# Optimization experiments

Hardware: AMD Instinct MI355X
Metric: run time of the kernel (lower is better)

The kernel has to match this reference:

```python
import jax, jax.numpy as jnp
import numpy as np

H = W = 128
BS = 16
# Ragged per-canvas stroke counts (sum = 2048)
LENGTHS = np.array([64, 192, 128, 96, 160, 224, 32, 128, 128, 256, 64, 96, 160, 128, 96, 96], dtype=np.int64)
L = int(LENGTHS.sum())


def setup_inputs() -> dict:
    key = jax.random.key(0)
    k1, k2, k3 = jax.random.split(key, 3)
    u = jax.random.uniform(k1, (L, 8), dtype=jnp.float32)
    # keep stroke width/height in [0.1, 0.6] so 1/w, 1/h stay well-conditioned
    strokes = u.at[:, 2:4].set(0.1 + 0.5 * u[:, 2:4])
    meta_brushes = jax.random.uniform(k2, (2, 1, H, W), dtype=jnp.float32)
    start_canvas = jax.random.uniform(k3, (BS, 3, H, W), dtype=jnp.float32)
    return {"strokes": strokes, "meta_brushes": meta_brushes,
            "start_canvas": start_canvas, "lengths": LENGTHS}


def _grid_sample_bilinear(img, gx, gy):
    """torch.nn.functional.grid_sample(mode='bilinear', padding_mode='zeros',
    align_corners=False) for single-channel images.
    img: [L, H, W]; gx, gy: [L, Ho, Wo] normalized coords in [-1, 1]."""
    Lb, Hi, Wi = img.shape
    ix = (gx + 1.0) * (Wi * 0.5) - 0.5
    iy = (gy + 1.0) * (Hi * 0.5) - 0.5
    x0 = jnp.floor(ix)
    y0 = jnp.floor(iy)
    x1 = x0 + 1.0
    y1 = y0 + 1.0
    wx1 = ix - x0
    wx0 = 1.0 - wx1
    wy1 = iy - y0
    wy0 = 1.0 - wy1
    bidx = jnp.arange(Lb)[:, None, None]

    def tap(xf, yf):
        xi = jnp.clip(xf, 0, Wi - 1).astype(jnp.int32)
        yi = jnp.clip(yf, 0, Hi - 1).astype(jnp.int32)
        valid = (xf >= 0) & (xf <= Wi - 1) & (yf >= 0) & (yf <= Hi - 1)
        return jnp.where(valid, img[bidx, yi, xi], 0.0)

    return (wy0 * wx0 * tap(x0, y0) + wy0 * wx1 * tap(x1, y0)
            + wy1 * wx0 * tap(x0, y1) + wy1 * wx1 * tap(x1, y1))


def _strokes2brushes(strokes, meta_brushes):
    """Per-stroke affine warp of the meta brush (affine_grid + grid_sample)."""
    x0, y0, w, h, theta = [strokes[:, i] for i in range(5)]
    colors = strokes[:, 5:8]  # [L, 3]
    idx = (h <= w).astype(jnp.int32)          # vertical vs horizontal brush
    imgs = meta_brushes[idx, 0]               # [L, H, W]

    rad = theta * jnp.pi
    s, c = jnp.sin(rad), jnp.cos(rad)
    w00 = c / w
    w01 = s * H / (W * w)
    w02 = (1 - 2 * x0) * w00 + (1 - 2 * y0) * w01
    w10 = -s * W / (H * h)
    w11 = c / h
    w12 = (1 - 2 * y0) * w11 - (1 - 2 * x0) * (-w10)

    # affine_grid(align_corners=False): pixel-center normalized coords
    xs = (2.0 * jnp.arange(W) + 1.0) / W - 1.0  # [W]
    ys = (2.0 * jnp.arange(H) + 1.0) / H - 1.0  # [H]
    gxb, gyb = jnp.meshgrid(xs, ys)             # [H, W] each
    gx = w00[:, None, None] * gxb + w01[:, None, None] * gyb + w02[:, None, None]
    gy = w10[:, None, None] * gxb + w11[:, None, None] * gyb + w12[:, None, None]

    brushes = _grid_sample_bilinear(imgs, gx, gy)  # [L, H, W]
    return colors, brushes


def _forward(strokes, meta_brushes, start_canvas, lengths):
    lengths = np.asarray(lengths)
    bs = len(lengths)
    colors, brushes = _strokes2brushes(strokes, meta_brushes)
    alphas = jnp.where(brushes <= 0.6, brushes, 1.0)  # [L, H, W]

    # Segmented reverse-cumsum (flip->cumsum->flip minus self), vectorized:
    # suffix_excl_i = seg_total - inclusive_prefix_i
    ends = np.cumsum(lengths)                 # [bs]
    starts = ends - lengths                   # [bs]
    seg = np.repeat(np.arange(bs), lengths)   # [L] static segment ids
    csum = jnp.cumsum(alphas, axis=0)         # [L, H, W]
    csum_pad = jnp.concatenate([jnp.zeros((1, H, W), csum.dtype), csum], axis=0)
    pre = csum_pad[starts]                    # [bs, H, W] cumsum before seg start
    totals = csum_pad[ends] - pre             # [bs, H, W] per-segment alpha sum
    suffix_excl = totals[seg] - (csum - pre[seg])

    b = jnp.clip(brushes - suffix_excl, 0.0, 1.0)  # [L, H, W]
    canvas = jax.ops.segment_sum(colors[:, :, None, None] * b[:, None],
                                 seg, num_segments=bs)  # [bs, 3, H, W]
    canvas_alpha = jnp.clip(totals, 0.0, 1.0)           # [bs, H, W]

    # F.interpolate to (H, W) is identity here (start_canvas already HxW)
    canvas = canvas + start_canvas * (1.0 - canvas_alpha[:, None])
    return canvas.astype(jnp.float32)


def reference(strokes, meta_brushes, start_canvas, lengths):
    return _forward(strokes, meta_brushes, start_canvas, lengths)
```

## Files before the change

kernel.cpp:

```cpp
#include <hip/hip_runtime.h>

#define HW_ 16384
#define BS_ 16

static __device__ __constant__ int g_start[BS_] = {
    0, 64, 256, 384, 480, 640, 864, 896,
    1024, 1152, 1408, 1472, 1568, 1728, 1856, 1952};
static __device__ __constant__ int g_len[BS_] = {
    64, 192, 128, 96, 160, 224, 32, 128,
    128, 256, 64, 96, 160, 128, 96, 96};
static __device__ __constant__ int g_perm[BS_] = {
    9, 5, 1, 12, 4, 2, 7, 8, 0, 3, 11, 13, 6, 10, 14, 15};

__global__ __launch_bounds__(256) void light_render_kernel(
    const float* __restrict__ strokes,
    const float* __restrict__ meta,
    const float* __restrict__ start_canvas,
    float* __restrict__ out)
{
    __shared__ float sc[256 * 12];
    __shared__ unsigned short slist[4 * 256];
    __shared__ int s_wcnt[4];

    const int b    = g_perm[blockIdx.x >> 6];
    const int tile = blockIdx.x & 63;
    const int tx = tile & 7, ty = tile >> 3;
    const int t    = threadIdx.x;
    const int lane = t & 63, wid = t >> 6;
    const int qx = wid & 1, qy = wid >> 1;
    const int c0p = (tx << 4) + (qx << 3);
    const int r0p = (ty << 4) + (qy << 3);
    const int col = c0p + (lane & 7);
    const int row = r0p + (lane >> 3);
    const int p   = (row << 7) + col;
    const int sg0 = g_start[b];
    const int len = g_len[b];

    const float cxb = (float)(32 * tx + 16) * 0.0078125f - 1.0f;
    const float cyb = (float)(32 * ty + 16) * 0.0078125f - 1.0f;
    const float exb = 15.0f / 128.0f;

    float d0=0,d1=0,d2=0,d3=0,d4=0,d5=0,d6=0,d7=0,d8=0,d9=0;
    bool keep = false;
    if (t < len) {
        const float4* sp = (const float4*)(strokes + (size_t)(sg0 + t) * 8);
        const float4 s0 = sp[0];
        const float4 s1 = sp[1];
        float sn, cs;
        sincosf(s1.x * 3.14159274101257324f, &sn, &cs);
        const float iw = 64.0f / s0.z;
        const float ih = 64.0f / s0.w;
        const float W00 = cs * iw, W01 = sn * iw;
        const float W10 = -sn * ih, W11 = cs * ih;
        const float ax = 1.0f - 2.0f * s0.x;
        const float ay = 1.0f - 2.0f * s0.y;
        const float W02 = fmaf(ax, W00, fmaf(ay, W01, 63.5f));
        const float W12 = fmaf(ay, W11, fmaf(ax, W10, 63.5f));
        const float cx = fmaf(W00, cxb, fmaf(W01, cyb, W02));
        const float cy = fmaf(W10, cxb, fmaf(W11, cyb, W12));
        const float rx = fabsf(W00) * exb + fabsf(W01) * exb;
        const float ry = fabsf(W10) * exb + fabsf(W11) * exb;
        keep = (fabsf(cx - 63.5f) <= 65.5f + rx) &&
               (fabsf(cy - 63.5f) <= 65.5f + ry);
        d0 = W00; d1 = W01; d2 = W02; d3 = W10; d4 = W11; d5 = W12;
        d6 = s1.y; d7 = s1.z; d8 = s1.w;
        d9 = (s0.w <= s0.z) ? 16384.0f : 0.0f;
    }
    const unsigned long long ball = __ballot(keep);
    const int pre = __popcll(ball & ((1ull << lane) - 1ull));
    if (lane == 0) s_wcnt[wid] = __popcll(ball);
    __syncthreads();
    int woff = 0;
    #pragma unroll
    for (int i = 0; i < 3; ++i) woff += (i < wid) ? s_wcnt[i] : 0;
    const int total = s_wcnt[0] + s_wcnt[1] + s_wcnt[2] + s_wcnt[3];
    if (keep) {
        float* dst = sc + (size_t)(woff + pre) * 12;
        dst[0]=d0; dst[1]=d1; dst[2]=d2;  dst[3]=d3; dst[4]=d4;  dst[5]=d5;
        dst[6]=d6; dst[7]=d7; dst[8]=d8;  dst[9]=d9; dst[10]=0.f; dst[11]=0.f;
    }
    __syncthreads();

    const float4* sv = (const float4*)sc;
    const float wcx = (float)(2 * c0p + 8) * 0.0078125f - 1.0f;
    const float wcy = (float)(2 * r0p + 8) * 0.0078125f - 1.0f;
    const float wex = 7.0f / 128.0f;
    unsigned short* wl = slist + (wid << 8);
    int wn = 0;
    for (int base = 0; base < total; base += 64) {
        const int k = base + lane;
        bool kp = false;
        if (k < total) {
            const float4 a0 = sv[k * 3];
            const float4 a1 = sv[k * 3 + 1];
            const float cx = fmaf(a0.x, wcx, fmaf(a0.y, wcy, a0.z));
            const float cy = fmaf(a0.w, wcx, fmaf(a1.x, wcy, a1.y));
            const float rx = fabsf(a0.x) * wex + fabsf(a0.y) * wex;
            const float ry = fabsf(a0.w) * wex + fabsf(a1.x) * wex;
            kp = (fabsf(cx - 63.5f) <= 65.5f + rx) &&
                 (fabsf(cy - 63.5f) <= 65.5f + ry);
        }
        const unsigned long long bl = __ballot(kp);
        if (kp) {
            const int pr = __popcll(bl & ((1ull << lane) - 1ull));
            wl[wn + pr] = (unsigned short)k;
        }
        wn += __popcll(bl);
    }

    const float gxb = (float)(2 * col + 1) * 0.0078125f - 1.0f;
    const float gyb = (float)(2 * row + 1) * 0.0078125f - 1.0f;

    float accR = 0.0f, accG = 0.0f, accB = 0.0f;
    float S = 0.0f;

    int j = wn - 1;
    float4 a0, a1, a2;
    if (j >= 0) {
        const int k = wl[j];
        a0 = sv[k*3]; a1 = sv[k*3+1]; a2 = sv[k*3+2];
    }
    while (j >= 0) {
        const int jn = j - 1;
        int kn = 0;
        if (jn >= 0) kn = wl[jn];
        const float4 c0 = a0, c1 = a1, c2 = a2;
        if (jn >= 0) {
            a0 = sv[kn*3]; a1 = sv[kn*3+1]; a2 = sv[kn*3+2];
        }

        const float ixf = fmaf(c0.x, gxb, fmaf(c0.y, gyb, c0.z));
        const float iyf = fmaf(c0.w, gxb, fmaf(c1.x, gyb, c1.y));
        const bool inside = (ixf > -1.0f) && (ixf < 128.0f) &&
                            (iyf > -1.0f) && (iyf < 128.0f);
        if (inside && (S < 1.0f)) {
            const float x0f = floorf(ixf), y0f = floorf(iyf);
            float wx1 = ixf - x0f, wy1 = iyf - y0f;
            float wx0 = 1.0f - wx1, wy0 = 1.0f - wy1;
            if (x0f < 0.0f)    wx0 = 0.0f;
            if (x0f > 126.0f)  wx1 = 0.0f;
            if (y0f < 0.0f)    wy0 = 0.0f;
            if (y0f > 126.0f)  wy1 = 0.0f;

            const int ix0 = (int)x0f, iy0 = (int)y0f;
            const int xi0 = max(ix0, 0), xi1 = min(ix0 + 1, 127);
            const int yi0 = max(iy0, 0), yi1 = min(iy0 + 1, 127);

            const float* img = meta + (int)c2.y;
            const int row0 = yi0 << 7, row1 = yi1 << 7;
            const float t00 = img[row0 + xi0];
            const float t01 = img[row0 + xi1];
            const float t10 = img[row1 + xi0];
            const float t11 = img[row1 + xi1];

            const float v = wy0 * fmaf(wx0, t00, wx1 * t01) +
                            wy1 * fmaf(wx0, t10, wx1 * t11);

            const float alpha = (v <= 0.6f) ? v : 1.0f;
            const float bb = fminf(fmaxf(v - S, 0.0f), 1.0f);
            accR = fmaf(c1.z, bb, accR);
            accG = fmaf(c1.w, bb, accG);
            accB = fmaf(c2.x, bb, accB);
            S += alpha;
        }
        if (__all(S >= 1.0f)) break;
        j = jn;
    }

    const float rem = 1.0f - fminf(S, 1.0f);
    const size_t base = ((size_t)b * 3) << 14;
    out[base + p]          = fmaf(start_canvas[base + p],          rem, accR);
    out[base + HW_ + p]    = fmaf(start_canvas[base + HW_ + p],    rem, accG);
    out[base + 2*HW_ + p]  = fmaf(start_canvas[base + 2*HW_ + p],  rem, accB);
}

extern "C" void kernel_launch(void* const* d_in, const int* in_sizes, int n_in,
                              void* d_out, int out_size, void* d_ws, size_t ws_size,
                              hipStream_t stream) {
    const float* strokes      = (const float*)d_in[0];
    const float* meta_brushes = (const float*)d_in[1];
    const float* start_canvas = (const float*)d_in[2];
    float* out = (float*)d_out;

    dim3 grid(BS_ * 64);
    dim3 block(256);
    light_render_kernel<<<grid, block, 0, stream>>>(strokes, meta_brushes,
                                                    start_canvas, out);
}
```

Measured before the change: 14.56 us.

## Precompute zero-padded 2x2 quad texture to fetch bilinear taps in one load

```diff
diff --git a/kernel.cpp b/kernel.cpp
--- a/kernel.cpp
+++ b/kernel.cpp
@@ -2,6 +2,8 @@
 
 #define HW_ 16384
 #define BS_ 16
+#define QW_ 129
+#define QIMG_ (QW_ * QW_)
 
 static __device__ __constant__ int g_start[BS_] = {
     0, 64, 256, 384, 480, 640, 864, 896,
@@ -12,9 +14,29 @@
 static __device__ __constant__ int g_perm[BS_] = {
     9, 5, 1, 12, 4, 2, 7, 8, 0, 3, 11, 13, 6, 10, 14, 15};
 
+__global__ __launch_bounds__(256) void quad_meta_kernel(
+    const float* __restrict__ meta, float4* __restrict__ Q)
+{
+    int i = blockIdx.x * 256 + threadIdx.x;
+    if (i >= 2 * QIMG_) return;
+    const int img = i / QIMG_, rem = i - img * QIMG_;
+    const int y = rem / QW_, x = rem - y * QW_;
+    const float* M = meta + img * HW_;
+    float q00 = 0.f, q01 = 0.f, q10 = 0.f, q11 = 0.f;
+    const bool rin0 = (y >= 1) && (y <= 128);
+    const bool rin1 = (y + 1 >= 1) && (y + 1 <= 128);
+    const bool cin0 = (x >= 1) && (x <= 128);
+    const bool cin1 = (x + 1 >= 1) && (x + 1 <= 128);
+    if (rin0 && cin0) q00 = M[((y - 1) << 7) + (x - 1)];
+    if (rin0 && cin1) q01 = M[((y - 1) << 7) + x];
+    if (rin1 && cin0) q10 = M[(y << 7) + (x - 1)];
+    if (rin1 && cin1) q11 = M[(y << 7) + x];
+    Q[i] = make_float4(q00, q01, q10, q11);
+}
+
 __global__ __launch_bounds__(256) void light_render_kernel(
     const float* __restrict__ strokes,
-    const float* __restrict__ meta,
+    const float4* __restrict__ Q,
     const float* __restrict__ start_canvas,
     float* __restrict__ out)
 {
@@ -64,7 +86,7 @@
                (fabsf(cy - 63.5f) <= 65.5f + ry);
         d0 = W00; d1 = W01; d2 = W02; d3 = W10; d4 = W11; d5 = W12;
         d6 = s1.y; d7 = s1.z; d8 = s1.w;
-        d9 = (s0.w <= s0.z) ? 16384.0f : 0.0f;
+        d9 = (s0.w <= s0.z) ? (float)QIMG_ : 0.0f;
     }
     const unsigned long long ball = __ballot(keep);
     const int pre = __popcll(ball & ((1ull << lane) - 1ull));
@@ -135,26 +157,12 @@
                             (iyf > -1.0f) && (iyf < 128.0f);
         if (inside && (S < 1.0f)) {
             const float x0f = floorf(ixf), y0f = floorf(iyf);
-            float wx1 = ixf - x0f, wy1 = iyf - y0f;
-            float wx0 = 1.0f - wx1, wy0 = 1.0f - wy1;
-            if (x0f < 0.0f)    wx0 = 0.0f;
-            if (x0f > 126.0f)  wx1 = 0.0f;
-            if (y0f < 0.0f)    wy0 = 0.0f;
-            if (y0f > 126.0f)  wy1 = 0.0f;
-
-            const int ix0 = (int)x0f, iy0 = (int)y0f;
-            const int xi0 = max(ix0, 0), xi1 = min(ix0 + 1, 127);
-            const int yi0 = max(iy0, 0), yi1 = min(iy0 + 1, 127);
-
-            const float* img = meta + (int)c2.y;
-            const int row0 = yi0 << 7, row1 = yi1 << 7;
-            const float t00 = img[row0 + xi0];
-            const float t01 = img[row0 + xi1];
-            const float t10 = img[row1 + xi0];
-            const float t11 = img[row1 + xi1];
-
-            const float v = wy0 * fmaf(wx0, t00, wx1 * t01) +
-                            wy1 * fmaf(wx0, t10, wx1 * t11);
+            const float wx1 = ixf - x0f, wy1 = iyf - y0f;
+            const float wx0 = 1.0f - wx1, wy0 = 1.0f - wy1;
+            const int xb = (int)x0f + 1, yb = (int)y0f + 1;
+            const float4 q = Q[(int)c2.y + yb * QW_ + xb];
+            const float v = wy0 * fmaf(wx0, q.x, wx1 * q.y) +
+                            wy1 * fmaf(wx0, q.z, wx1 * q.w);
 
             const float alpha = (v <= 0.6f) ? v : 1.0f;
             const float bb = fminf(fmaxf(v - S, 0.0f), 1.0f);
@@ -180,10 +188,13 @@
     const float* strokes      = (const float*)d_in[0];
     const float* meta_brushes = (const float*)d_in[1];
     const float* start_canvas = (const float*)d_in[2];
-    float* out = (float*)d_out;
+    float*  out = (float*)d_out;
+    float4* Qws = (float4*)d_ws;
+
+    quad_meta_kernel<<<(2 * QIMG_ + 255) / 256, 256, 0, stream>>>(meta_brushes, Qws);
 
     dim3 grid(BS_ * 64);
     dim3 block(256);
-    light_render_kernel<<<grid, block, 0, stream>>>(strokes, meta_brushes,
+    light_render_kernel<<<grid, block, 0, stream>>>(strokes, Qws,
                                                     start_canvas, out);
 }
```

Result: slower. 18.39 us (+26.3%).

## Split stroke sequence across waves with per-round alpha prefix exchange

Applied to the files above, without the earlier changes.

```diff
diff --git a/kernel.cpp b/kernel.cpp
--- a/kernel.cpp
+++ b/kernel.cpp
@@ -2,6 +2,7 @@
 
 #define HW_ 16384
 #define BS_ 16
+#define K_  16
 
 static __device__ __constant__ int g_start[BS_] = {
     0, 64, 256, 384, 480, 640, 864, 896,
@@ -10,7 +11,9 @@
     64, 192, 128, 96, 160, 224, 32, 128,
     128, 256, 64, 96, 160, 128, 96, 96};
 static __device__ __constant__ int g_perm[BS_] = {
-    9, 5, 1, 12, 4, 2, 7, 8, 0, 3, 11, 13, 6, 10, 14, 15};
+    9, 0, 4, 1, 12, 5, 2, 7, 3, 8, 11, 10, 14, 13, 6, 15};
+static __device__ __constant__ int g_txor[8] = {
+    0x00, 0x33, 0x55, 0x66, 0x99, 0xAA, 0xCC, 0xFF};
 
 __global__ __launch_bounds__(256) void light_render_kernel(
     const float* __restrict__ strokes,
@@ -18,29 +21,28 @@
     const float* __restrict__ start_canvas,
     float* __restrict__ out)
 {
-    __shared__ float sc[256 * 12];
-    __shared__ unsigned short slist[4 * 256];
-    __shared__ int s_wcnt[4];
+    __shared__ float4 sgeo[256 * 2];
+    __shared__ float4 scol[256];
+    __shared__ int    s_wcnt[4];
+    __shared__ float  sS[4][64];
+    __shared__ float  sAcc[4][64 * 3];
 
-    const int b    = g_perm[blockIdx.x >> 6];
-    const int tile = blockIdx.x & 63;
-    const int tx = tile & 7, ty = tile >> 3;
-    const int t    = threadIdx.x;
-    const int lane = t & 63, wid = t >> 6;
-    const int qx = wid & 1, qy = wid >> 1;
-    const int c0p = (tx << 4) + (qx << 3);
-    const int r0p = (ty << 4) + (qy << 3);
-    const int col = c0p + (lane & 7);
-    const int row = r0p + (lane >> 3);
+    const int bi   = blockIdx.x;
+    const int b    = g_perm[bi >> 8];
+    const int tile = (bi & 255) ^ g_txor[(bi >> 9) & 7];
+    const int tx = tile & 15, ty = tile >> 4;
+    const int t = threadIdx.x, lane = t & 63, wid = t >> 6;
+    const int col = (tx << 3) + (lane & 7);
+    const int row = (ty << 3) + (lane >> 3);
     const int p   = (row << 7) + col;
     const int sg0 = g_start[b];
     const int len = g_len[b];
 
-    const float cxb = (float)(32 * tx + 16) * 0.0078125f - 1.0f;
-    const float cyb = (float)(32 * ty + 16) * 0.0078125f - 1.0f;
-    const float exb = 15.0f / 128.0f;
+    const float cxb = (float)(16 * tx + 8) * 0.0078125f - 1.0f;
+    const float cyb = (float)(16 * ty + 8) * 0.0078125f - 1.0f;
+    const float exb = 7.0f / 128.0f;
 
-    float d0=0,d1=0,d2=0,d3=0,d4=0,d5=0,d6=0,d7=0,d8=0,d9=0;
+    float4 e0 = make_float4(0.f, 0.f, 0.f, 0.f), e1 = e0, e2 = e0;
     bool keep = false;
     if (t < len) {
         const float4* sp = (const float4*)(strokes + (size_t)(sg0 + t) * 8);
@@ -62,9 +64,9 @@
         const float ry = fabsf(W10) * exb + fabsf(W11) * exb;
         keep = (fabsf(cx - 63.5f) <= 65.5f + rx) &&
                (fabsf(cy - 63.5f) <= 65.5f + ry);
-        d0 = W00; d1 = W01; d2 = W02; d3 = W10; d4 = W11; d5 = W12;
-        d6 = s1.y; d7 = s1.z; d8 = s1.w;
-        d9 = (s0.w <= s0.z) ? 16384.0f : 0.0f;
+        e0 = make_float4(W00, W01, W02, W10);
+        e1 = make_float4(W11, W12, (s0.w <= s0.z) ? 16384.0f : 0.0f, 0.f);
+        e2 = make_float4(s1.y, s1.z, s1.w, 0.f);
     }
     const unsigned long long ball = __ballot(keep);
     const int pre = __popcll(ball & ((1ull << lane) - 1ull));
@@ -75,103 +77,104 @@
     for (int i = 0; i < 3; ++i) woff += (i < wid) ? s_wcnt[i] : 0;
     const int total = s_wcnt[0] + s_wcnt[1] + s_wcnt[2] + s_wcnt[3];
     if (keep) {
-        float* dst = sc + (size_t)(woff + pre) * 12;
-        dst[0]=d0; dst[1]=d1; dst[2]=d2;  dst[3]=d3; dst[4]=d4;  dst[5]=d5;
-        dst[6]=d6; dst[7]=d7; dst[8]=d8;  dst[9]=d9; dst[10]=0.f; dst[11]=0.f;
+        const int d = woff + pre;
+        sgeo[2 * d] = e0;
+        sgeo[2 * d + 1] = e1;
+        scol[d] = e2;
     }
     __syncthreads();
-
-    const float4* sv = (const float4*)sc;
-    const float wcx = (float)(2 * c0p + 8) * 0.0078125f - 1.0f;
-    const float wcy = (float)(2 * r0p + 8) * 0.0078125f - 1.0f;
-    const float wex = 7.0f / 128.0f;
-    unsigned short* wl = slist + (wid << 8);
-    int wn = 0;
-    for (int base = 0; base < total; base += 64) {
-        const int k = base + lane;
-        bool kp = false;
-        if (k < total) {
-            const float4 a0 = sv[k * 3];
-            const float4 a1 = sv[k * 3 + 1];
-            const float cx = fmaf(a0.x, wcx, fmaf(a0.y, wcy, a0.z));
-            const float cy = fmaf(a0.w, wcx, fmaf(a1.x, wcy, a1.y));
-            const float rx = fabsf(a0.x) * wex + fabsf(a0.y) * wex;
-            const float ry = fabsf(a0.w) * wex + fabsf(a1.x) * wex;
-            kp = (fabsf(cx - 63.5f) <= 65.5f + rx) &&
-                 (fabsf(cy - 63.5f) <= 65.5f + ry);
-        }
-        const unsigned long long bl = __ballot(kp);
-        if (kp) {
-            const int pr = __popcll(bl & ((1ull << lane) - 1ull));
-            wl[wn + pr] = (unsigned short)k;
-        }
-        wn += __popcll(bl);
-    }
 
     const float gxb = (float)(2 * col + 1) * 0.0078125f - 1.0f;
     const float gyb = (float)(2 * row + 1) * 0.0078125f - 1.0f;
 
-    float accR = 0.0f, accG = 0.0f, accB = 0.0f;
-    float S = 0.0f;
+    float accR = 0.f, accG = 0.f, accB = 0.f;
+    float Scar = 0.f;
+    const int rounds = (total + 4 * K_ - 1) / (4 * K_);
 
-    int j = wn - 1;
-    float4 a0, a1, a2;
-    if (j >= 0) {
-        const int k = wl[j];
-        a0 = sv[k*3]; a1 = sv[k*3+1]; a2 = sv[k*3+2];
-    }
-    while (j >= 0) {
-        const int jn = j - 1;
-        int kn = 0;
-        if (jn >= 0) kn = wl[jn];
-        const float4 c0 = a0, c1 = a1, c2 = a2;
-        if (jn >= 0) {
-            a0 = sv[kn*3]; a1 = sv[kn*3+1]; a2 = sv[kn*3+2];
+    for (int r = 0; r < rounds; ++r) {
+        const int pbase = r * (4 * K_) + wid * K_;
+        float v[K_];
+        float sa = 0.f;
+        #pragma unroll
+        for (int s = 0; s < K_; ++s) {
+            float vs = 0.f;
+            const int pos = pbase + s;
+            if (pos < total) {
+                const int j = total - 1 - pos;
+                const float4 c0 = sgeo[2 * j];
+                const float4 c1 = sgeo[2 * j + 1];
+                const float ixf = fmaf(c0.x, gxb, fmaf(c0.y, gyb, c0.z));
+                const float iyf = fmaf(c0.w, gxb, fmaf(c1.x, gyb, c1.y));
+                const bool inside = (ixf > -1.0f) && (ixf < 128.0f) &&
+                                    (iyf > -1.0f) && (iyf < 128.0f);
+                if (inside) {
+                    const float x0f = floorf(ixf), y0f = floorf(iyf);
+                    float wx1 = ixf - x0f, wy1 = iyf - y0f;
+                    float wx0 = 1.0f - wx1, wy0 = 1.0f - wy1;
+                    if (x0f < 0.0f)    wx0 = 0.0f;
+                    if (x0f > 126.0f)  wx1 = 0.0f;
+                    if (y0f < 0.0f)    wy0 = 0.0f;
+                    if (y0f > 126.0f)  wy1 = 0.0f;
+                    const int ix0 = (int)x0f, iy0 = (int)y0f;
+                    const int xi0 = max(ix0, 0), xi1 = min(ix0 + 1, 127);
+                    const int yi0 = max(iy0, 0), yi1 = min(iy0 + 1, 127);
+                    const float* img = meta + (int)c1.z;
+                    const int r0 = yi0 << 7, r1 = yi1 << 7;
+                    const float t00 = img[r0 + xi0];
+                    const float t01 = img[r0 + xi1];
+                    const float t10 = img[r1 + xi0];
+                    const float t11 = img[r1 + xi1];
+                    vs = wy0 * fmaf(wx0, t00, wx1 * t01) +
+                         wy1 * fmaf(wx0, t10, wx1 * t11);
+                }
+            }
+            v[s] = vs;
+            sa += (vs <= 0.6f) ? vs : 1.0f;
         }
-
-        const float ixf = fmaf(c0.x, gxb, fmaf(c0.y, gyb, c0.z));
-        const float iyf = fmaf(c0.w, gxb, fmaf(c1.x, gyb, c1.y));
-        const bool inside = (ixf > -1.0f) && (ixf < 128.0f) &&
-                            (iyf > -1.0f) && (iyf < 128.0f);
-        if (inside && (S < 1.0f)) {
-            const float x0f = floorf(ixf), y0f = floorf(iyf);
-            float wx1 = ixf - x0f, wy1 = iyf - y0f;
-            float wx0 = 1.0f - wx1, wy0 = 1.0f - wy1;
-            if (x0f < 0.0f)    wx0 = 0.0f;
-            if (x0f > 126.0f)  wx1 = 0.0f;
-            if (y0f < 0.0f)    wy0 = 0.0f;
-            if (y0f > 126.0f)  wy1 = 0.0f;
-
-            const int ix0 = (int)x0f, iy0 = (int)y0f;
-            const int xi0 = max(ix0, 0), xi1 = min(ix0 + 1, 127);
-            const int yi0 = max(iy0, 0), yi1 = min(iy0 + 1, 127);
-
-            const float* img = meta + (int)c2.y;
-            const int row0 = yi0 << 7, row1 = yi1 << 7;
-            const float t00 = img[row0 + xi0];
-            const float t01 = img[row0 + xi1];
-            const float t10 = img[row1 + xi0];
-            const float t11 = img[row1 + xi1];
-
-            const float v = wy0 * fmaf(wx0, t00, wx1 * t01) +
-                            wy1 * fmaf(wx0, t10, wx1 * t11);
-
-            const float alpha = (v <= 0.6f) ? v : 1.0f;
-            const float bb = fminf(fmaxf(v - S, 0.0f), 1.0f);
-            accR = fmaf(c1.z, bb, accR);
-            accG = fmaf(c1.w, bb, accG);
-            accB = fmaf(c2.x, bb, accB);
-            S += alpha;
+        sS[wid][lane] = sa;
+        __syncthreads();
+        float S = Scar;
+        if (wid > 0) S += sS[0][lane];
+        if (wid > 1) S += sS[1][lane];
+        if (wid > 2) S += sS[2][lane];
+        const float Sall = Scar + sS[0][lane] + sS[1][lane] +
+                                  sS[2][lane] + sS[3][lane];
+        #pragma unroll
+        for (int s = 0; s < K_; ++s) {
+            const int pos = pbase + s;
+            if (pos < total) {
+                const int j = total - 1 - pos;
+                const float4 cc = scol[j];
+                const float vs = v[s];
+                const float bb = fminf(fmaxf(vs - S, 0.0f), 1.0f);
+                accR = fmaf(cc.x, bb, accR);
+                accG = fmaf(cc.y, bb, accG);
+                accB = fmaf(cc.z, bb, accB);
+                S += (vs <= 0.6f) ? vs : 1.0f;
+            }
         }
-        if (__all(S >= 1.0f)) break;
-        j = jn;
+        __syncthreads();
+        Scar = Sall;
+        if (__all(Scar >= 1.0f)) break;
     }
 
-    const float rem = 1.0f - fminf(S, 1.0f);
-    const size_t base = ((size_t)b * 3) << 14;
-    out[base + p]          = fmaf(start_canvas[base + p],          rem, accR);
-    out[base + HW_ + p]    = fmaf(start_canvas[base + HW_ + p],    rem, accG);
-    out[base + 2*HW_ + p]  = fmaf(start_canvas[base + 2*HW_ + p],  rem, accB);
+    sAcc[wid][lane * 3 + 0] = accR;
+    sAcc[wid][lane * 3 + 1] = accG;
+    sAcc[wid][lane * 3 + 2] = accB;
+    __syncthreads();
+    if (wid == 0) {
+        const float aR = sAcc[0][lane*3+0] + sAcc[1][lane*3+0] +
+                         sAcc[2][lane*3+0] + sAcc[3][lane*3+0];
+        const float aG = sAcc[0][lane*3+1] + sAcc[1][lane*3+1] +
+                         sAcc[2][lane*3+1] + sAcc[3][lane*3+1];
+        const float aB = sAcc[0][lane*3+2] + sAcc[1][lane*3+2] +
+                         sAcc[2][lane*3+2] + sAcc[3][lane*3+2];
+        const float rem = 1.0f - fminf(Scar, 1.0f);
+        const size_t base = ((size_t)b * 3) << 14;
+        out[base + p]           = fmaf(start_canvas[base + p],           rem, aR);
+        out[base + HW_ + p]     = fmaf(start_canvas[base + HW_ + p],     rem, aG);
+        out[base + 2*HW_ + p]   = fmaf(start_canvas[base + 2*HW_ + p],   rem, aB);
+    }
 }
 
 extern "C" void kernel_launch(void* const* d_in, const int* in_sizes, int n_in,
@@ -182,7 +185,7 @@
     const float* start_canvas = (const float*)d_in[2];
     float* out = (float*)d_out;
 
-    dim3 grid(BS_ * 64);
+    dim3 grid(BS_ * 256);
     dim3 block(256);
     light_render_kernel<<<grid, block, 0, stream>>>(strokes, meta_brushes,
                                                     start_canvas, out);
```

After: 27.69 us. 1.9x slower.
